# Kernel tuning notes

Hardware: AMD Instinct MI355X
Metric: run time of the kernel (lower is better)

The kernel has to match this reference:

```python
import jax, jax.numpy as jnp
import numpy as np

N = 100000
E = 1600000
IN_F = 128
OUT_F = 64
ALPHA = 0.2  # leaky relu negative slope


def setup_inputs() -> dict:
    key = jax.random.key(0)
    k1, k2, k3, k4, k5, k6 = jax.random.split(key, 6)
    x = jax.random.normal(k1, (N, IN_F), dtype=jnp.float32)
    # xavier_uniform with gain=1.414
    limit_W = 1.414 * np.sqrt(6.0 / (IN_F + OUT_F))
    W = jax.random.uniform(k2, (IN_F, OUT_F), minval=-limit_W, maxval=limit_W, dtype=jnp.float32)
    limit_a = 1.414 * np.sqrt(6.0 / (OUT_F + 1))
    a_left = jax.random.uniform(k3, (OUT_F,), minval=-limit_a, maxval=limit_a, dtype=jnp.float32)
    a_right = jax.random.uniform(k4, (OUT_F,), minval=-limit_a, maxval=limit_a, dtype=jnp.float32)
    edge_index = jax.random.randint(k5, (2, E), 0, N, dtype=jnp.int64)
    return {"x": x, "W": W, "a_left": a_left, "a_right": a_right, "edge_index": edge_index}


def reference(x, W, a_left, a_right, edge_index):
    src = edge_index[0]  # [E] destination rows of scatter (attention normalized per src)
    dst = edge_index[1]  # [E] neighbor features gathered
    Wh = x @ W                      # [N, OUT_F]
    e_left = Wh @ a_left            # [N]
    e_right = Wh @ a_right          # [N]
    e = e_left[src] + e_right[dst]  # [E]
    e = jnp.where(e > 0, e, ALPHA * e)  # leaky relu
    # segment softmax over edges grouped by src
    e_max = jax.ops.segment_max(e, src, num_segments=N)   # [N]
    e_exp = jnp.exp(e - e_max[src])                        # [E]
    e_sum = jax.ops.segment_sum(e_exp, src, num_segments=N)  # [N]
    alpha = e_exp / (e_sum[src] + 1e-9)                    # [E]
    messages = alpha[:, None] * Wh[dst]                    # [E, OUT_F]
    out = jax.ops.segment_sum(messages, src, num_segments=N)  # [N, OUT_F]
    return jax.nn.relu(out)
```

## Files before the change

### kernel.cpp

```cpp
#include <hip/hip_runtime.h>

#define IN_F 128
#define OUT_F 64
#define NEG_SLOPE 0.2f
#define NBLK 256
#define LCAP 4096

__device__ __forceinline__ unsigned short f2bf(float f) {
    unsigned u = __float_as_uint(f);
    unsigned r = (u + 0x7FFFu + ((u >> 16) & 1u)) >> 16;
    return (unsigned short)r;
}
__device__ __forceinline__ float bf2f(unsigned short b) {
    return __uint_as_float(((unsigned)b) << 16);
}

__global__ void __launch_bounds__(256) gemm_tiled(
    const float* __restrict__ x, const float* __restrict__ W,
    const float* __restrict__ a_l, const float* __restrict__ a_r,
    unsigned short* __restrict__ Whb, float* __restrict__ el, float* __restrict__ er,
    int N)
{
    __shared__ float xs[64][132];
    __shared__ float Ws[128][64];

    const int t = threadIdx.x;
    const int row0 = blockIdx.x * 64;

    {
        const float4* Wsrc = (const float4*)W;
        float4* Wd = (float4*)(&Ws[0][0]);
#pragma unroll
        for (int i = 0; i < 8; ++i) Wd[t + 256 * i] = Wsrc[t + 256 * i];
    }
    {
        int r = t >> 5;
        int c = (t & 31) * 4;
#pragma unroll
        for (int i = 0; i < 8; ++i) {
            int rr = r + 8 * i;
            int grow = row0 + rr;
            float4 v = make_float4(0.f, 0.f, 0.f, 0.f);
            if (grow < N) v = *(const float4*)(x + (size_t)grow * IN_F + c);
            xs[rr][c] = v.x; xs[rr][c + 1] = v.y; xs[rr][c + 2] = v.z; xs[rr][c + 3] = v.w;
        }
    }
    __syncthreads();

    const int tx = t & 15, ty = t >> 4;
    float acc[4][4] = {};

#pragma unroll 2
    for (int kk = 0; kk < 32; ++kk) {
        float4 xv[4];
#pragma unroll
        for (int i = 0; i < 4; ++i) xv[i] = *(const float4*)&xs[4 * ty + i][4 * kk];
#pragma unroll
        for (int kc = 0; kc < 4; ++kc) {
            float4 wv = *(const float4*)&Ws[4 * kk + kc][4 * tx];
#pragma unroll
            for (int i = 0; i < 4; ++i) {
                float xe = (kc == 0) ? xv[i].x : (kc == 1) ? xv[i].y : (kc == 2) ? xv[i].z : xv[i].w;
                acc[i][0] = fmaf(xe, wv.x, acc[i][0]);
                acc[i][1] = fmaf(xe, wv.y, acc[i][1]);
                acc[i][2] = fmaf(xe, wv.z, acc[i][2]);
                acc[i][3] = fmaf(xe, wv.w, acc[i][3]);
            }
        }
    }

    float4 al4 = ((const float4*)a_l)[tx];
    float4 ar4 = ((const float4*)a_r)[tx];

#pragma unroll
    for (int i = 0; i < 4; ++i) {
        int grow = row0 + 4 * ty + i;
        if (grow < N) {
            ushort4 o;
            o.x = f2bf(acc[i][0]); o.y = f2bf(acc[i][1]);
            o.z = f2bf(acc[i][2]); o.w = f2bf(acc[i][3]);
            *(ushort4*)(Whb + (size_t)grow * OUT_F + 4 * tx) = o;
        }
        float pl = acc[i][0] * al4.x + acc[i][1] * al4.y + acc[i][2] * al4.z + acc[i][3] * al4.w;
        float pr = acc[i][0] * ar4.x + acc[i][1] * ar4.y + acc[i][2] * ar4.z + acc[i][3] * ar4.w;
#pragma unroll
        for (int off = 1; off < 16; off <<= 1) {
            pl += __shfl_xor(pl, off);
            pr += __shfl_xor(pr, off);
        }
        if (tx == 0 && grow < N) { el[grow] = pl; er[grow] = pr; }
    }
}

__global__ void __launch_bounds__(256) countA(
    const int* __restrict__ src, int* __restrict__ hist2d, int E, int EPB, int NBUCK)
{
    extern __shared__ int h[];
    for (int i = threadIdx.x; i < NBUCK; i += 256) h[i] = 0;
    __syncthreads();
    const int b = blockIdx.x;
    const int e0 = b * EPB, e1 = min(e0 + EPB, E);
    for (int e = e0 + threadIdx.x; e < e1; e += 256)
        atomicAdd(&h[src[e] >> 6], 1);
    __syncthreads();
    for (int i = threadIdx.x; i < NBUCK; i += 256) hist2d[i * NBLK + b] = h[i];
}

__global__ void __launch_bounds__(256) sumB(
    const int* __restrict__ hist2d, int* __restrict__ total, int NBUCK)
{
    const int w = (blockIdx.x * blockDim.x + threadIdx.x) >> 6;
    const int lane = threadIdx.x & 63;
    if (w >= NBUCK) return;
    int4 v = ((const int4*)(hist2d + (size_t)w * NBLK))[lane];
    int s = v.x + v.y + v.z + v.w;
#pragma unroll
    for (int o = 32; o; o >>= 1) s += __shfl_xor(s, o);
    if (lane == 0) total[w] = s;
}

__global__ void __launch_bounds__(256) scanS(
    const int* __restrict__ total, int* __restrict__ bbase, int* __restrict__ row_ptr,
    int NBUCK, int N, int E)
{
    __shared__ int wsum[4];
    const int t = threadIdx.x, lane = t & 63, wid = t >> 6;
    const int CH = (NBUCK + 255) / 256;
    int loc[32];
    int s = 0;
    for (int i = 0; i < CH && i < 32; ++i) {
        int idx = t * CH + i;
        int v = (idx < NBUCK) ? total[idx] : 0;
        loc[i] = v; s += v;
    }
    int incl = s;
#pragma unroll
    for (int o = 1; o < 64; o <<= 1) {
        int x = __shfl_up(incl, o);
        if (lane >= o) incl += x;
    }
    if (lane == 63) wsum[wid] = incl;
    __syncthreads();
    int wbase = 0;
    for (int k = 0; k < wid; ++k) wbase += wsum[k];
    int run = wbase + incl - s;
    for (int i = 0; i < CH && i < 32; ++i) {
        int idx = t * CH + i;
        if (idx < NBUCK) bbase[idx] = run;
        run += loc[i];
    }
    if (t == 0) { bbase[NBUCK] = E; row_ptr[N] = E; }
}

__global__ void __launch_bounds__(256) scanBB(
    const int* __restrict__ hist2d, const int* __restrict__ bbase,
    int* __restrict__ offsets, int NBUCK)
{
    const int w = (blockIdx.x * blockDim.x + threadIdx.x) >> 6;
    const int lane = threadIdx.x & 63;
    if (w >= NBUCK) return;
    int4 v = ((const int4*)(hist2d + (size_t)w * NBLK))[lane];
    int s1 = v.x, s2 = s1 + v.y, s3 = s2 + v.z, s4 = s3 + v.w;
    int incl = s4;
#pragma unroll
    for (int o = 1; o < 64; o <<= 1) {
        int x = __shfl_up(incl, o);
        if (lane >= o) incl += x;
    }
    int base = bbase[w] + incl - s4;
    offsets[(size_t)(4 * lane + 0) * NBUCK + w] = base;
    offsets[(size_t)(4 * lane + 1) * NBUCK + w] = base + s1;
    offsets[(size_t)(4 * lane + 2) * NBUCK + w] = base + s2;
    offsets[(size_t)(4 * lane + 3) * NBUCK + w] = base + s3;
}

__global__ void __launch_bounds__(256) binB(
    const int* __restrict__ src, const int* __restrict__ dst,
    const int* __restrict__ offsets, unsigned* __restrict__ rec,
    int E, int EPB, int NBUCK)
{
    extern __shared__ int sh[];
    int* off = sh;
    int* cnt = sh + NBUCK;
    const int b = blockIdx.x;
    for (int i = threadIdx.x; i < NBUCK; i += 256) {
        off[i] = offsets[(size_t)b * NBUCK + i];
        cnt[i] = 0;
    }
    __syncthreads();
    const int e0 = b * EPB, e1 = min(e0 + EPB, E);
    for (int e = e0 + threadIdx.x; e < e1; e += 256) {
        int s = src[e];
        int j = s >> 6;
        int r = atomicAdd(&cnt[j], 1);
        rec[off[j] + r] = ((unsigned)dst[e] << 6) | (unsigned)(s & 63);
    }
}

__global__ void __launch_bounds__(256) buckz(
    const unsigned* __restrict__ rec, const float* __restrict__ er,
    const int* __restrict__ bbase, int* __restrict__ row_ptr,
    int* __restrict__ sdst, float* __restrict__ serv, int N, int NBUCK)
{
    __shared__ unsigned recs[LCAP];
    __shared__ int cnt[64], cur[64];
    const int j = blockIdx.x;
    const int t = threadIdx.x;
    const int s0 = bbase[j], s1 = bbase[j + 1];
    const int len = s1 - s0;
    const bool lds = (len <= LCAP);

    if (t < 64) cnt[t] = 0;
    __syncthreads();
    for (int i = t; i < len; i += 256) {
        unsigned r = rec[s0 + i];
        if (lds) recs[i] = r;
        atomicAdd(&cnt[r & 63u], 1);
    }
    __syncthreads();
    if (t < 64) {
        int v = cnt[t];
        int incl = v;
#pragma unroll
        for (int o = 1; o < 64; o <<= 1) {
            int x = __shfl_up(incl, o);
            if (t >= o) incl += x;
        }
        cur[t] = incl - v;
        int node = j * 64 + t;
        if (node < N) row_ptr[node] = s0 + incl - v;
    }
    __syncthreads();
    for (int i = t; i < len; i += 256) {
        unsigned r = lds ? recs[i] : rec[s0 + i];
        int s6 = (int)(r & 63u);
        int d  = (int)(r >> 6);
        int p  = atomicAdd(&cur[s6], 1);
        sdst[s0 + p] = d;
        serv[s0 + p] = er[d];
    }
}

__global__ void __launch_bounds__(256) node_k(
    const int* __restrict__ row_ptr, const int* __restrict__ sdst,
    const float* __restrict__ serv, const float* __restrict__ el,
    const unsigned short* __restrict__ Whb, float* __restrict__ out, int N)
{
    const int lane = threadIdx.x & 63;
    const int node = (blockIdx.x * blockDim.x + threadIdx.x) >> 6;
    if (node >= N) return;

    const int start = row_ptr[node], end = row_ptr[node + 1];
    const float elc = el[node];

    float m = -1e30f;
    for (int base = start; base < end; base += 64) {
        int idx = base + lane;
        if (idx < end) {
            float v = elc + serv[idx];
            v = v > 0.f ? v : NEG_SLOPE * v;
            m = fmaxf(m, v);
        }
    }
#pragma unroll
    for (int off = 32; off; off >>= 1) m = fmaxf(m, __shfl_xor(m, off));

    float Z = 0.f, acc = 0.f;
    for (int base = start; base < end; base += 64) {
        int idx = base + lane;
        int cnt = min(64, end - base);
        float p = 0.f;
        int d = 0;
        if (idx < end) {
            d = sdst[idx];
            float v = elc + serv[idx];
            v = v > 0.f ? v : NEG_SLOPE * v;
            p = __expf(v - m);
        }
        Z += p;
        for (int jj = 0; jj < cnt; ++jj) {
            int dj = __shfl(d, jj);
            float pj = __shfl(p, jj);
            acc = fmaf(pj, bf2f(Whb[(size_t)dj * OUT_F + lane]), acc);
        }
    }
#pragma unroll
    for (int off = 32; off; off >>= 1) Z += __shfl_xor(Z, off);

    out[(size_t)node * OUT_F + lane] = fmaxf(acc / (Z + 1e-9f), 0.f);
}

extern "C" void kernel_launch(void* const* d_in, const int* in_sizes, int n_in,
                              void* d_out, int out_size, void* d_ws, size_t ws_size,
                              hipStream_t stream)
{
    const float* x   = (const float*)d_in[0];
    const float* W   = (const float*)d_in[1];
    const float* a_l = (const float*)d_in[2];
    const float* a_r = (const float*)d_in[3];
    const int*   ei  = (const int*)d_in[4];

    const int N = in_sizes[0] / IN_F;
    const int E = in_sizes[4] / 2;
    const int* src = ei;
    const int* dst = ei + E;
    float* out = (float*)d_out;

    const int NBUCK = (N + 63) >> 6;
    const int EPB = (E + NBLK - 1) / NBLK;

    auto align = [](size_t v) { return (v + 255) & ~(size_t)255; };
    char* ws = (char*)d_ws;
    size_t off = 0;
    unsigned short* Whb = (unsigned short*)(ws + off); off = align(off + (size_t)N * OUT_F * 2);
    float* el      = (float*)(ws + off);   off = align(off + (size_t)N * 4);
    float* er      = (float*)(ws + off);   off = align(off + (size_t)N * 4);
    unsigned* rec  = (unsigned*)(ws + off);off = align(off + (size_t)E * 4);
    int* hist2d    = (int*)(ws + off);     off = align(off + (size_t)NBUCK * NBLK * 4);
    int* offsets   = (int*)(ws + off);     off = align(off + (size_t)NBUCK * NBLK * 4);
    int* total     = (int*)(ws + off);     off = align(off + (size_t)NBUCK * 4);
    int* bbase     = (int*)(ws + off);     off = align(off + (size_t)(NBUCK + 1) * 4);
    int* row_ptr   = (int*)(ws + off);     off = align(off + (size_t)(N + 1) * 4);
    int* sdst      = (int*)(ws + off);     off = align(off + (size_t)E * 4);
    float* serv    = (float*)(ws + off);   off = align(off + (size_t)E * 4);

    gemm_tiled<<<(N + 63) / 64, 256, 0, stream>>>(x, W, a_l, a_r, Whb, el, er, N);

    countA<<<NBLK, 256, NBUCK * 4, stream>>>(src, hist2d, E, EPB, NBUCK);
    sumB  <<<(NBUCK + 3) / 4, 256, 0, stream>>>(hist2d, total, NBUCK);
    scanS <<<1, 256, 0, stream>>>(total, bbase, row_ptr, NBUCK, N, E);
    scanBB<<<(NBUCK + 3) / 4, 256, 0, stream>>>(hist2d, bbase, offsets, NBUCK);
    binB  <<<NBLK, 256, (size_t)NBUCK * 8, stream>>>(src, dst, offsets, rec, E, EPB, NBUCK);
    buckz <<<NBUCK, 256, 0, stream>>>(rec, er, bbase, row_ptr, sdst, serv, N, NBUCK);

    node_k<<<(N * 64 + 255) / 256, 256, 0, stream>>>(row_ptr, sdst, serv, el, Whb, out, N);
}
```

Baseline: 314.1 us.

## Fuse bucket sort and per-node aggregation into one bucket-level LDS-atomic kernel

Replaces the buckz local sort (which wrote row_ptr, sdst and serv) and the per-node node_k aggregation with one kernel, buckagg. It works straight from the bucketed edge records and accumulates exp-weights and weighted Wh rows into shared-memory accumulators using LDS atomics. This removes a full sort pass and the E-sized sdst/serv writes and re-reads, plus one launch. The segment max subtraction is also dropped, so exp(e) is computed unshifted, which risks overflow for large logits. It adds LDS float-atomic traffic and 32KB+ of shared memory per block.

```diff
diff --git a/kernel.cpp b/kernel.cpp
--- a/kernel.cpp
+++ b/kernel.cpp
@@ -120,8 +120,7 @@
 }
 
 __global__ void __launch_bounds__(256) scanS(
-    const int* __restrict__ total, int* __restrict__ bbase, int* __restrict__ row_ptr,
-    int NBUCK, int N, int E)
+    const int* __restrict__ total, int* __restrict__ bbase, int NBUCK, int E)
 {
     __shared__ int wsum[4];
     const int t = threadIdx.x, lane = t & 63, wid = t >> 6;
@@ -149,7 +148,7 @@
         if (idx < NBUCK) bbase[idx] = run;
         run += loc[i];
     }
-    if (t == 0) { bbase[NBUCK] = E; row_ptr[N] = E; }
+    if (t == 0) bbase[NBUCK] = E;
 }
 
 __global__ void __launch_bounds__(256) scanBB(
@@ -197,97 +196,68 @@
     }
 }
 
-__global__ void __launch_bounds__(256) buckz(
-    const unsigned* __restrict__ rec, const float* __restrict__ er,
-    const int* __restrict__ bbase, int* __restrict__ row_ptr,
-    int* __restrict__ sdst, float* __restrict__ serv, int N, int NBUCK)
-{
-    __shared__ unsigned recs[LCAP];
-    __shared__ int cnt[64], cur[64];
+__global__ void __launch_bounds__(256) buckagg(
+    const unsigned* __restrict__ rec, const float* __restrict__ el,
+    const float* __restrict__ er, const unsigned short* __restrict__ Whb,
+    const int* __restrict__ bbase, float* __restrict__ out, int N)
+{
+    __shared__ float p_s[LCAP];
+    __shared__ float acc_s[64 * 64];
+    __shared__ float Z_s[64];
+    __shared__ float el_s[64];
+
     const int j = blockIdx.x;
     const int t = threadIdx.x;
     const int s0 = bbase[j], s1 = bbase[j + 1];
     const int len = s1 - s0;
-    const bool lds = (len <= LCAP);
-
-    if (t < 64) cnt[t] = 0;
-    __syncthreads();
-    for (int i = t; i < len; i += 256) {
-        unsigned r = rec[s0 + i];
-        if (lds) recs[i] = r;
-        atomicAdd(&cnt[r & 63u], 1);
-    }
-    __syncthreads();
+    const int node0 = j * 64;
+
     if (t < 64) {
-        int v = cnt[t];
-        int incl = v;
-#pragma unroll
-        for (int o = 1; o < 64; o <<= 1) {
-            int x = __shfl_up(incl, o);
-            if (t >= o) incl += x;
-        }
-        cur[t] = incl - v;
-        int node = j * 64 + t;
-        if (node < N) row_ptr[node] = s0 + incl - v;
-    }
-    __syncthreads();
-    for (int i = t; i < len; i += 256) {
-        unsigned r = lds ? recs[i] : rec[s0 + i];
-        int s6 = (int)(r & 63u);
-        int d  = (int)(r >> 6);
-        int p  = atomicAdd(&cur[s6], 1);
-        sdst[s0 + p] = d;
-        serv[s0 + p] = er[d];
-    }
-}
-
-__global__ void __launch_bounds__(256) node_k(
-    const int* __restrict__ row_ptr, const int* __restrict__ sdst,
-    const float* __restrict__ serv, const float* __restrict__ el,
-    const unsigned short* __restrict__ Whb, float* __restrict__ out, int N)
-{
-    const int lane = threadIdx.x & 63;
-    const int node = (blockIdx.x * blockDim.x + threadIdx.x) >> 6;
-    if (node >= N) return;
-
-    const int start = row_ptr[node], end = row_ptr[node + 1];
-    const float elc = el[node];
-
-    float m = -1e30f;
-    for (int base = start; base < end; base += 64) {
-        int idx = base + lane;
-        if (idx < end) {
-            float v = elc + serv[idx];
+        int node = node0 + t;
+        el_s[t] = (node < N) ? el[node] : 0.f;
+        Z_s[t] = 0.f;
+    }
+    for (int i = t; i < 64 * 64; i += 256) acc_s[i] = 0.f;
+    __syncthreads();
+
+    const int lane = t & 63;
+    const int wid = t >> 6;
+
+    for (int c0 = 0; c0 < len; c0 += LCAP) {
+        const int clen = min(LCAP, len - c0);
+
+        for (int i = t; i < clen; i += 256) {
+            unsigned r = rec[s0 + c0 + i];
+            int d  = (int)(r >> 6);
+            int s6 = (int)(r & 63u);
+            float v = el_s[s6] + er[d];
             v = v > 0.f ? v : NEG_SLOPE * v;
-            m = fmaxf(m, v);
-        }
-    }
-#pragma unroll
-    for (int off = 32; off; off >>= 1) m = fmaxf(m, __shfl_xor(m, off));
-
-    float Z = 0.f, acc = 0.f;
-    for (int base = start; base < end; base += 64) {
-        int idx = base + lane;
-        int cnt = min(64, end - base);
-        float p = 0.f;
-        int d = 0;
-        if (idx < end) {
-            d = sdst[idx];
-            float v = elc + serv[idx];
-            v = v > 0.f ? v : NEG_SLOPE * v;
-            p = __expf(v - m);
-        }
-        Z += p;
-        for (int jj = 0; jj < cnt; ++jj) {
-            int dj = __shfl(d, jj);
-            float pj = __shfl(p, jj);
-            acc = fmaf(pj, bf2f(Whb[(size_t)dj * OUT_F + lane]), acc);
-        }
-    }
-#pragma unroll
-    for (int off = 32; off; off >>= 1) Z += __shfl_xor(Z, off);
-
-    out[(size_t)node * OUT_F + lane] = fmaxf(acc / (Z + 1e-9f), 0.f);
+            float p = __expf(v);
+            p_s[i] = p;
+            atomicAdd(&Z_s[s6], p);
+        }
+        __syncthreads();
+
+        for (int i = wid; i < clen; i += 4) {
+            unsigned r = rec[s0 + c0 + i];
+            int d  = (int)(r >> 6);
+            int s6 = (int)(r & 63u);
+            float p = p_s[i];
+            float wh = bf2f(Whb[(size_t)d * OUT_F + lane]);
+            atomicAdd(&acc_s[s6 * 64 + lane], p * wh);
+        }
+        __syncthreads();
+    }
+
+    for (int i = t; i < 64 * 64; i += 256) {
+        int s6 = i >> 6;
+        int node = node0 + s6;
+        if (node < N) {
+            float z = Z_s[s6];
+            float o = (z > 0.f) ? acc_s[i] / z : 0.f;
+            out[(size_t)node * OUT_F + (i & 63)] = fmaxf(o, 0.f);
+        }
+    }
 }
 
 extern "C" void kernel_launch(void* const* d_in, const int* in_sizes, int n_in,
@@ -320,18 +290,14 @@
     int* offsets   = (int*)(ws + off);     off = align(off + (size_t)NBUCK * NBLK * 4);
     int* total     = (int*)(ws + off);     off = align(off + (size_t)NBUCK * 4);
     int* bbase     = (int*)(ws + off);     off = align(off + (size_t)(NBUCK + 1) * 4);
-    int* row_ptr   = (int*)(ws + off);     off = align(off + (size_t)(N + 1) * 4);
-    int* sdst      = (int*)(ws + off);     off = align(off + (size_t)E * 4);
-    float* serv    = (float*)(ws + off);   off = align(off + (size_t)E * 4);
 
     gemm_tiled<<<(N + 63) / 64, 256, 0, stream>>>(x, W, a_l, a_r, Whb, el, er, N);
 
     countA<<<NBLK, 256, NBUCK * 4, stream>>>(src, hist2d, E, EPB, NBUCK);
     sumB  <<<(NBUCK + 3) / 4, 256, 0, stream>>>(hist2d, total, NBUCK);
-    scanS <<<1, 256, 0, stream>>>(total, bbase, row_ptr, NBUCK, N, E);
+    scanS <<<1, 256, 0, stream>>>(total, bbase, NBUCK, E);
     scanBB<<<(NBUCK + 3) / 4, 256, 0, stream>>>(hist2d, bbase, offsets, NBUCK);
     binB  <<<NBLK, 256, (size_t)NBUCK * 8, stream>>>(src, dst, offsets, rec, E, EPB, NBUCK);
-    buckz <<<NBUCK, 256, 0, stream>>>(rec, er, bbase, row_ptr, sdst, serv, N, NBUCK);
-
-    node_k<<<(N * 64 + 255) / 256, 256, 0, stream>>>(row_ptr, sdst, serv, el, Whb, out, N);
-}
+
+    buckagg<<<NBUCK, 256, 0, stream>>>(rec, el, er, Whb, bbase, out, N);
+}
```

After: 808.3 us. 2.57x slower.
